# Kernel optimization log

Hardware: AMD Instinct MI355X
Metric: run time of the kernel (lower is better)

## Reference

```python
import jax, jax.numpy as jnp
import numpy as np

BATCH, C, BOX = 8, 1, 160
N, L = 20, 20


def setup_inputs() -> dict:
    key = jax.random.key(0)
    k1, k2, k3 = jax.random.split(key, 3)
    x = jax.random.normal(k1, (BATCH, C, BOX, BOX), dtype=jnp.float32)
    basis = jax.random.normal(k2, (N, L, 2, BOX, BOX), dtype=jnp.float32)
    angles = jax.random.uniform(k3, (BATCH,), dtype=jnp.float32) * (2.0 * np.pi)
    return {"x": x, "basis": basis, "angles": angles}


def reference(x, basis, angles):
    # euclid2basis: linear basis projection (GEMM in disguise)
    # coeffs: [b, c, N, L, 2]
    coeffs = jnp.einsum('bcij,nlrij->bcnlr', x, basis)

    # rotate: complex rotation of angular modes, angle scaled by harmonic index l
    l_mult = jnp.arange(L, dtype=x.dtype)                  # [L]
    ang = angles[:, None, None, None] * l_mult             # [b, 1, 1, L]
    ca, sa = jnp.cos(ang), jnp.sin(ang)
    a = coeffs[..., 0] * ca + coeffs[..., 1] * sa
    b = coeffs[..., 1] * ca - coeffs[..., 0] * sa
    rot = jnp.stack([a, b], axis=-1)                       # [b, c, N, L, 2]

    # basis2euclid: reconstruction (transpose GEMM)
    out = jnp.einsum('bcnlr,nlrij->bcij', rot, basis)      # [b, c, H, W]
    return out
```

## Files before the change

### kernel.cpp

```cpp
#include <hip/hip_runtime.h>
#include <math.h>

#define BATCH   8
#define LDIM    20
#define PIX     25600
#define PIX4    6400
#define NLPAIRS 400
#define NLR     800

#define NLG     2
#define KSPLIT  5
#define SLICE   (PIX4 / KSPLIT)

#define CHUNKS    8
#define CHUNK_NLR 100

__global__ __launch_bounds__(256) void proj_kernel(
    const float* __restrict__ x,
    const float* __restrict__ basis,
    float* __restrict__ coeffs)
{
    const int tid   = threadIdx.x;
    const int rbase = blockIdx.x * (NLG * 2);
    const int kbase = blockIdx.y * SLICE;

    const float4* __restrict__ r0 = (const float4*)(basis + (size_t)(rbase + 0) * PIX);
    const float4* __restrict__ r1 = (const float4*)(basis + (size_t)(rbase + 1) * PIX);
    const float4* __restrict__ r2 = (const float4*)(basis + (size_t)(rbase + 2) * PIX);
    const float4* __restrict__ r3 = (const float4*)(basis + (size_t)(rbase + 3) * PIX);
    const float4* __restrict__ x4 = (const float4*)x;

    float acc[4][BATCH];
    #pragma unroll
    for (int r = 0; r < 4; ++r)
        #pragma unroll
        for (int b = 0; b < BATCH; ++b) acc[r][b] = 0.0f;

    #pragma unroll
    for (int it = 0; it < SLICE / 256; ++it) {
        const int i = kbase + it * 256 + tid;
        float4 b0 = r0[i];
        float4 b1 = r1[i];
        float4 b2 = r2[i];
        float4 b3 = r3[i];
        #pragma unroll
        for (int b = 0; b < BATCH; ++b) {
            float4 xv = x4[(size_t)b * PIX4 + i];
            acc[0][b] = fmaf(b0.x, xv.x, acc[0][b]);
            acc[0][b] = fmaf(b0.y, xv.y, acc[0][b]);
            acc[0][b] = fmaf(b0.z, xv.z, acc[0][b]);
            acc[0][b] = fmaf(b0.w, xv.w, acc[0][b]);
            acc[1][b] = fmaf(b1.x, xv.x, acc[1][b]);
            acc[1][b] = fmaf(b1.y, xv.y, acc[1][b]);
            acc[1][b] = fmaf(b1.z, xv.z, acc[1][b]);
            acc[1][b] = fmaf(b1.w, xv.w, acc[1][b]);
            acc[2][b] = fmaf(b2.x, xv.x, acc[2][b]);
            acc[2][b] = fmaf(b2.y, xv.y, acc[2][b]);
            acc[2][b] = fmaf(b2.z, xv.z, acc[2][b]);
            acc[2][b] = fmaf(b2.w, xv.w, acc[2][b]);
            acc[3][b] = fmaf(b3.x, xv.x, acc[3][b]);
            acc[3][b] = fmaf(b3.y, xv.y, acc[3][b]);
            acc[3][b] = fmaf(b3.z, xv.z, acc[3][b]);
            acc[3][b] = fmaf(b3.w, xv.w, acc[3][b]);
        }
    }

    #pragma unroll
    for (int r = 0; r < 4; ++r)
        #pragma unroll
        for (int b = 0; b < BATCH; ++b)
            #pragma unroll
            for (int off = 32; off > 0; off >>= 1)
                acc[r][b] += __shfl_down(acc[r][b], off);

    __shared__ float red[4][32];
    const int wave = tid >> 6;
    const int lane = tid & 63;
    if (lane == 0) {
        #pragma unroll
        for (int r = 0; r < 4; ++r)
            #pragma unroll
            for (int b = 0; b < BATCH; ++b)
                red[wave][r * BATCH + b] = acc[r][b];
    }
    __syncthreads();

    if (tid < 32) {
        const int r = tid >> 3;
        const int b = tid & 7;
        float v = red[0][tid] + red[1][tid] + red[2][tid] + red[3][tid];
        atomicAdd(&coeffs[(size_t)(rbase + r) * BATCH + b], v);
    }
}

__global__ __launch_bounds__(256) void recon_kernel(
    const float* __restrict__ basis,
    const float* __restrict__ coeffs,
    const float* __restrict__ angles,
    float* __restrict__ out)
{
    __shared__ float rl[CHUNK_NLR * BATCH];

    const int tid = threadIdx.x;
    const int c0  = blockIdx.y * CHUNK_NLR;

    for (int idx = tid; idx < CHUNK_NLR * BATCH; idx += 256) {
        const int k   = idx >> 3;
        const int b   = idx & 7;
        const int nlr = c0 + k;
        const int r   = nlr & 1;
        const int l   = (nlr >> 1) % LDIM;
        float self  = coeffs[(size_t)nlr * BATCH + b];
        float other = coeffs[(size_t)(nlr ^ 1) * BATCH + b];
        float ang = angles[b] * (float)l;
        float ca, sa;
        __sincosf(ang, &sa, &ca);
        rl[idx] = r == 0 ? fmaf(self, ca, other * sa)
                         : fmaf(self, ca, -other * sa);
    }
    __syncthreads();

    const int pix = blockIdx.x * 256 + tid;

    float acc[BATCH];
    #pragma unroll
    for (int b = 0; b < BATCH; ++b) acc[b] = 0.0f;

    const float* __restrict__ bp = basis + (size_t)c0 * PIX + pix;

    #pragma unroll 5
    for (int k = 0; k < CHUNK_NLR; ++k) {
        float bv = bp[(size_t)k * PIX];
        float4 v0 = *(const float4*)&rl[k * BATCH];
        float4 v1 = *(const float4*)&rl[k * BATCH + 4];
        acc[0] = fmaf(bv, v0.x, acc[0]);
        acc[1] = fmaf(bv, v0.y, acc[1]);
        acc[2] = fmaf(bv, v0.z, acc[2]);
        acc[3] = fmaf(bv, v0.w, acc[3]);
        acc[4] = fmaf(bv, v1.x, acc[4]);
        acc[5] = fmaf(bv, v1.y, acc[5]);
        acc[6] = fmaf(bv, v1.z, acc[6]);
        acc[7] = fmaf(bv, v1.w, acc[7]);
    }

    #pragma unroll
    for (int b = 0; b < BATCH; ++b)
        atomicAdd(&out[(size_t)b * PIX + pix], acc[b]);
}

extern "C" void kernel_launch(void* const* d_in, const int* in_sizes, int n_in,
                              void* d_out, int out_size, void* d_ws, size_t ws_size,
                              hipStream_t stream) {
    (void)in_sizes; (void)n_in; (void)ws_size;

    const float* x      = (const float*)d_in[0];
    const float* basis  = (const float*)d_in[1];
    const float* angles = (const float*)d_in[2];
    float* out    = (float*)d_out;
    float* coeffs = (float*)d_ws;

    hipMemsetAsync(d_ws, 0, (size_t)NLR * BATCH * sizeof(float), stream);
    hipMemsetAsync(d_out, 0, (size_t)out_size * sizeof(float), stream);

    proj_kernel<<<dim3(NLPAIRS / NLG, KSPLIT), dim3(256), 0, stream>>>(x, basis, coeffs);
    recon_kernel<<<dim3(PIX / 256, CHUNKS), dim3(256), 0, stream>>>(basis, coeffs, angles, out);
}
```

Before: 45.61 us.

## Replace atomics and memsets with split-K partial buffers and in-block reduction

The projection kernel now writes per-K-slice partial coefficients to separate workspace slots instead of using atomicAdd, so the coeffs memset is no longer needed. The reconstruction kernel sums the partials, precomputes the sin/cos table once per block, and splits the NLR reduction across four waves with a shared-memory reduction. It then writes the output directly, which removes the output memset and the global atomics. In exchange, every recon block redundantly rebuilds all 800x8 rotated coefficients (reading 5 partials each), and there are fewer pixels per block (400 blocks).

```diff
diff --git a/kernel.cpp b/kernel.cpp
--- a/kernel.cpp
+++ b/kernel.cpp
@@ -12,13 +12,14 @@
 #define KSPLIT  5
 #define SLICE   (PIX4 / KSPLIT)
 
-#define CHUNKS    8
-#define CHUNK_NLR 100
+#define RPIX    64
+#define RKS     4
+#define RKLEN   (NLR / RKS)
 
 __global__ __launch_bounds__(256) void proj_kernel(
     const float* __restrict__ x,
     const float* __restrict__ basis,
-    float* __restrict__ coeffs)
+    float* __restrict__ part)
 {
     const int tid   = threadIdx.x;
     const int rbase = blockIdx.x * (NLG * 2);
@@ -89,50 +90,62 @@
         const int r = tid >> 3;
         const int b = tid & 7;
         float v = red[0][tid] + red[1][tid] + red[2][tid] + red[3][tid];
-        atomicAdd(&coeffs[(size_t)(rbase + r) * BATCH + b], v);
+        part[((size_t)blockIdx.y * NLR + rbase + r) * BATCH + b] = v;
     }
 }
 
 __global__ __launch_bounds__(256) void recon_kernel(
     const float* __restrict__ basis,
-    const float* __restrict__ coeffs,
+    const float* __restrict__ part,
     const float* __restrict__ angles,
     float* __restrict__ out)
 {
-    __shared__ float rl[CHUNK_NLR * BATCH];
+    __shared__ float rl[NLR * BATCH];
+    __shared__ float red[RKS - 1][RPIX][BATCH];
+    __shared__ float cst[LDIM * BATCH], snt[LDIM * BATCH];
 
     const int tid = threadIdx.x;
-    const int c0  = blockIdx.y * CHUNK_NLR;
 
-    for (int idx = tid; idx < CHUNK_NLR * BATCH; idx += 256) {
-        const int k   = idx >> 3;
-        const int b   = idx & 7;
-        const int nlr = c0 + k;
-        const int r   = nlr & 1;
-        const int l   = (nlr >> 1) % LDIM;
-        float self  = coeffs[(size_t)nlr * BATCH + b];
-        float other = coeffs[(size_t)(nlr ^ 1) * BATCH + b];
-        float ang = angles[b] * (float)l;
-        float ca, sa;
-        __sincosf(ang, &sa, &ca);
-        rl[idx] = r == 0 ? fmaf(self, ca, other * sa)
-                         : fmaf(self, ca, -other * sa);
+    if (tid < LDIM * BATCH) {
+        const int l = tid >> 3;
+        const int b = tid & 7;
+        __sincosf(angles[b] * (float)l, &snt[tid], &cst[tid]);
     }
     __syncthreads();
 
-    const int pix = blockIdx.x * 256 + tid;
+    for (int idx = tid; idx < NLR * BATCH; idx += 256) {
+        const int nlr = idx >> 3;
+        const int b   = idx & 7;
+        float self = 0.0f, other = 0.0f;
+        #pragma unroll
+        for (int s = 0; s < KSPLIT; ++s) {
+            self  += part[((size_t)s * NLR + nlr) * BATCH + b];
+            other += part[((size_t)s * NLR + (nlr ^ 1)) * BATCH + b];
+        }
+        const int l  = (nlr >> 1) % LDIM;
+        const float ca = cst[l * BATCH + b];
+        const float sa = snt[l * BATCH + b];
+        rl[idx] = (nlr & 1) == 0 ? fmaf(self, ca, other * sa)
+                                 : fmaf(self, ca, -other * sa);
+    }
+    __syncthreads();
+
+    const int lane = tid & 63;
+    const int ks   = tid >> 6;
+    const int pix  = blockIdx.x * RPIX + lane;
 
     float acc[BATCH];
     #pragma unroll
     for (int b = 0; b < BATCH; ++b) acc[b] = 0.0f;
 
-    const float* __restrict__ bp = basis + (size_t)c0 * PIX + pix;
+    const float* __restrict__ bp = basis + (size_t)(ks * RKLEN) * PIX + pix;
+    const float* __restrict__ rp = &rl[(ks * RKLEN) * BATCH];
 
-    #pragma unroll 5
-    for (int k = 0; k < CHUNK_NLR; ++k) {
+    #pragma unroll 10
+    for (int k = 0; k < RKLEN; ++k) {
         float bv = bp[(size_t)k * PIX];
-        float4 v0 = *(const float4*)&rl[k * BATCH];
-        float4 v1 = *(const float4*)&rl[k * BATCH + 4];
+        float4 v0 = *(const float4*)&rp[k * BATCH];
+        float4 v1 = *(const float4*)&rp[k * BATCH + 4];
         acc[0] = fmaf(bv, v0.x, acc[0]);
         acc[1] = fmaf(bv, v0.y, acc[1]);
         acc[2] = fmaf(bv, v0.z, acc[2]);
@@ -143,25 +156,36 @@
         acc[7] = fmaf(bv, v1.w, acc[7]);
     }
 
-    #pragma unroll
-    for (int b = 0; b < BATCH; ++b)
-        atomicAdd(&out[(size_t)b * PIX + pix], acc[b]);
+    if (ks > 0) {
+        #pragma unroll
+        for (int b = 0; b < BATCH; ++b)
+            red[ks - 1][lane][b] = acc[b];
+    }
+    __syncthreads();
+
+    if (ks == 0) {
+        #pragma unroll
+        for (int w = 0; w < RKS - 1; ++w)
+            #pragma unroll
+            for (int b = 0; b < BATCH; ++b)
+                acc[b] += red[w][lane][b];
+        #pragma unroll
+        for (int b = 0; b < BATCH; ++b)
+            out[(size_t)b * PIX + pix] = acc[b];
+    }
 }
 
 extern "C" void kernel_launch(void* const* d_in, const int* in_sizes, int n_in,
                               void* d_out, int out_size, void* d_ws, size_t ws_size,
                               hipStream_t stream) {
-    (void)in_sizes; (void)n_in; (void)ws_size;
+    (void)in_sizes; (void)n_in; (void)ws_size; (void)out_size;
 
     const float* x      = (const float*)d_in[0];
     const float* basis  = (const float*)d_in[1];
     const float* angles = (const float*)d_in[2];
-    float* out    = (float*)d_out;
-    float* coeffs = (float*)d_ws;
+    float* out  = (float*)d_out;
+    float* part = (float*)d_ws;
 
-    hipMemsetAsync(d_ws, 0, (size_t)NLR * BATCH * sizeof(float), stream);
-    hipMemsetAsync(d_out, 0, (size_t)out_size * sizeof(float), stream);
-
-    proj_kernel<<<dim3(NLPAIRS / NLG, KSPLIT), dim3(256), 0, stream>>>(x, basis, coeffs);
-    recon_kernel<<<dim3(PIX / 256, CHUNKS), dim3(256), 0, stream>>>(basis, coeffs, angles, out);
+    proj_kernel<<<dim3(NLPAIRS / NLG, KSPLIT), dim3(256), 0, stream>>>(x, basis, part);
+    recon_kernel<<<dim3(PIX / RPIX), dim3(256), 0, stream>>>(basis, part, angles, out);
 }
```

New measurement: 42.12 us. -7.7%, faster.
